# Kernel optimization log

Hardware: AMD Instinct MI355X
Metric: run time of the kernel (lower is better)

## Reference

```python
import jax, jax.numpy as jnp
import numpy as np

M, B, N, NUM_CLASSES = 3, 16, 512, 12
IOU_THR = 0.5


def setup_inputs() -> dict:
    key = jax.random.key(0)
    k1, k2, k3, k4, k5 = jax.random.split(key, 5)
    # Valid xyxy boxes in a ~1024x1024 image: x2>x1, y2>y1
    xy = jax.random.uniform(k1, (M, B, N, 2)) * 900.0
    wh = jax.random.uniform(k2, (M, B, N, 2)) * 120.0 + 4.0
    boxes = jnp.concatenate([xy, xy + wh], axis=-1)
    scores = jax.random.uniform(k3, (M, B, N))
    labels = jax.random.randint(k4, (M, B, N), 0, NUM_CLASSES)
    w = jax.random.uniform(k5, (M,)) + 0.5
    weights = w / jnp.sum(w)  # module normalizes weights to sum to 1
    return {"boxes": boxes, "scores": scores, "labels": labels, "weights": weights}


def _pairwise_iou(b):
    # b: [K,4] xyxy -> [K,K] IoU
    x1, y1, x2, y2 = b[:, 0], b[:, 1], b[:, 2], b[:, 3]
    area = (x2 - x1) * (y2 - y1)
    iw = jnp.clip(jnp.minimum(x2[:, None], x2[None, :]) - jnp.maximum(x1[:, None], x1[None, :]), 0.0)
    ih = jnp.clip(jnp.minimum(y2[:, None], y2[None, :]) - jnp.maximum(y1[:, None], y1[None, :]), 0.0)
    inter = iw * ih
    union = area[:, None] + area[None, :] - inter
    return inter / jnp.maximum(union, 1e-9)


def _nms_one_image(boxes, scores, labels):
    # boxes [K,4], scores [K], labels [K] -> [K,5] (kept boxes + kept score, suppressed rows zeroed)
    K = boxes.shape[0]
    order = jnp.argsort(-scores)  # descending score, like torchvision.ops.nms
    b = boxes[order]
    s = scores[order]
    l = labels[order]
    iou = _pairwise_iou(b)  # [K,K]
    # class-aware: only same-label boxes can suppress each other (per-label NMS loop in the original)
    suppress = (iou > IOU_THR) & (l[:, None] == l[None, :])
    idx = jnp.arange(K)
    def body(i, keep):
        # box i is suppressed iff a higher-scoring kept box of the same label overlaps > thr
        conflict = jnp.any(suppress[i] & keep & (idx < i))
        return keep.at[i].set(jnp.logical_not(conflict))
    keep = jax.lax.fori_loop(0, K, body, jnp.ones((K,), dtype=bool))
    kf = keep.astype(b.dtype)
    return jnp.concatenate([b * kf[:, None], (s * kf)[:, None]], axis=-1)


def reference(boxes, scores, labels, weights):
    # Gather all models' detections per image with score weighting, then class-aware NMS.
    K = M * N
    b = jnp.transpose(boxes, (1, 0, 2, 3)).reshape(B, K, 4)
    s = jnp.transpose(scores * weights[:, None, None], (1, 0, 2)).reshape(B, K)
    l = jnp.transpose(labels, (1, 0, 2)).reshape(B, K)
    return jax.vmap(_nms_one_image)(b, s, l)  # [B, K, 5]
```

## Files before the change

### kernel.cpp

```cpp
#include <hip/hip_runtime.h>

#define MM 3
#define BB 16
#define NN 512
#define KK 1536
#define NCLS 12
#define LMAX 256
#define LW 4
#define NTHREADS 1024
#define NWAVES 16

__global__ __launch_bounds__(NTHREADS) void nms_fused_kernel(
    const float* __restrict__ boxes, const float* __restrict__ scores,
    const int* __restrict__ labels, const float* __restrict__ weights,
    float* __restrict__ out) {
#pragma clang fp contract(off)
  int cls = blockIdx.x, b = blockIdx.y;
  int tid = threadIdx.x, lane = tid & 63, wave = tid >> 6;

  __shared__ unsigned long long kl[KK];
  __shared__ unsigned long long mkey[LMAX + 2];
  __shared__ int memb[LMAX];
  __shared__ int wcnt[NWAVES];
  __shared__ int pr[8][128];
  __shared__ float4 lb[LMAX];
  __shared__ float lsc[LMAX];
  __shared__ unsigned short listR[LMAX];
  __shared__ unsigned long long mask[LMAX][LW];
  __shared__ unsigned long long kwS[LW];

  float w0 = weights[0], w1 = weights[1], w2 = weights[2];
  bool has1 = (wave < 8);
  int t0 = wave * 64 + lane;
  int t1 = (wave + 16) * 64 + lane;
  int m0i = t0 >> 9, n0i = t0 & 511;
  float s0 = scores[(m0i * BB + b) * NN + n0i];
  int l0 = labels[(m0i * BB + b) * NN + n0i];
  float s1 = 0.0f; int l1 = -1;
  if (has1) {
    int m1i = t1 >> 9, n1i = t1 & 511;
    s1 = scores[(m1i * BB + b) * NN + n1i];
    l1 = labels[(m1i * BB + b) * NN + n1i];
  }
  unsigned long long lmask = (1ULL << lane) - 1ULL;
  float wm0 = (m0i == 0) ? w0 : ((m0i == 1) ? w1 : w2);
  unsigned long long key0 =
      ((unsigned long long)(~__float_as_uint(s0 * wm0)) << 16) | (unsigned)t0;
  kl[t0] = key0;
  bool mem0 = (l0 == cls);
  unsigned long long bk0 = __ballot(mem0);
  int off0 = __popcll(bk0 & lmask);
  int wl = __popcll(bk0);
  unsigned long long key1 = 0ULL; bool mem1 = false; int off1 = 0;
  if (has1) {
    int m1i = t1 >> 9;
    float wm1 = (m1i == 0) ? w0 : ((m1i == 1) ? w1 : w2);
    key1 = ((unsigned long long)(~__float_as_uint(s1 * wm1)) << 16) |
           (unsigned)t1;
    kl[t1] = key1;
    mem1 = (l1 == cls);
    unsigned long long bk1 = __ballot(mem1);
    off1 = wl + __popcll(bk1 & lmask);
    wl += __popcll(bk1);
  }
  if (lane == 0) wcnt[wave] = wl;
  __syncthreads();
  int wbase = 0, L = 0;
#pragma unroll
  for (int w = 0; w < NWAVES; ++w) {
    if (w < wave) wbase += wcnt[w];
    L += wcnt[w];
  }
  if (L > LMAX) L = LMAX;
  if (mem0) {
    int p = wbase + off0;
    if (p < LMAX) { memb[p] = t0; mkey[p] = key0; }
  }
  if (mem1) {
    int p = wbase + off1;
    if (p < LMAX) { memb[p] = t1; mkey[p] = key1; }
  }
  if (tid < 2) mkey[L + tid] = ~0ULL;
  __syncthreads();

  const ulonglong2* k2 = (const ulonglong2*)kl;
  const ulonglong2* m2 = (const ulonglong2*)mkey;
  int nH = (L + 1) >> 1;
  int pidx = tid & 127, s = tid >> 7;
  for (int p0 = 0; p0 < L; p0 += 128) {
    int p = p0 + pidx;
    bool own = (s == 0) && (p < L);
    unsigned long long k0 = (p < L) ? mkey[p] : ~0ULL;
    float4 box = make_float4(0.f, 0.f, 0.f, 0.f);
    if (own) {
      int e = memb[p];
      box = ((const float4*)boxes)[((e >> 9) * BB + b) * NN + (e & 511)];
    }
    int r = 0;
    const ulonglong2* ks = k2 + s * (KK / 16);
#pragma unroll 8
    for (int j = 0; j < KK / 16; ++j) {
      ulonglong2 kk = ks[j];
      r += (int)(kk.x < k0) + (int)(kk.y < k0);
    }
    pr[s][pidx] = r;
    int lp = 0;
    if (own) {
      for (int q = 0; q < nH; ++q) {
        ulonglong2 mm = m2[q];
        lp += (int)(mm.x < k0) + (int)(mm.y < k0);
      }
    }
    __syncthreads();
    if (own) {
      int grank = pr[0][pidx] + pr[1][pidx] + pr[2][pidx] + pr[3][pidx] +
                  pr[4][pidx] + pr[5][pidx] + pr[6][pidx] + pr[7][pidx];
      lb[lp] = box;
      lsc[lp] = __uint_as_float(~(unsigned)(k0 >> 16));
      listR[lp] = (unsigned short)grank;
    }
    __syncthreads();
  }

  int nWd = (L + 63) >> 6;
  for (int v = 0; v < nWd; ++v) {
    int j = v * 64 + lane;
    float4 bj = lb[min(j, L - 1)];
    float aj = (bj.z - bj.x) * (bj.w - bj.y);
    for (int i = v * 64 + wave; i < L; i += NWAVES) {
      float4 bi = lb[i];
      float ai = (bi.z - bi.x) * (bi.w - bi.y);
      float iw = fminf(bi.z, bj.z) - fmaxf(bi.x, bj.x); iw = fmaxf(iw, 0.0f);
      float ih = fminf(bi.w, bj.w) - fmaxf(bi.y, bj.y); ih = fmaxf(ih, 0.0f);
      float inter = iw * ih;
      float uni = (ai + aj) - inter;
      bool sup = (j < i) && ((double)inter > (double)uni * (0.5 + 0x1p-25));
      unsigned long long bits = __ballot(sup);
      if (lane == 0) mask[i][v] = bits;
    }
  }
  __syncthreads();

  if (wave == 0) {
    for (int w = 0; w < nWd; ++w) {
      int row = w * 64 + lane;
      unsigned long long cp = 0ULL, sup = 0ULL;
      if (row < L) {
        for (int v = 0; v < w; ++v) cp |= mask[row][v] & kwS[v];
        sup = mask[row][w];
      }
      bool conf = (cp != 0ULL);
      unsigned long long Kb = 0ULL, Sb = 0ULL;
      while (true) {
        bool kill = conf || ((sup & Kb) != 0ULL);
        bool keep = !conf && ((sup & ~Sb) == 0ULL);
        Kb = __ballot(keep);
        Sb = __ballot(kill);
        if ((Kb | Sb) == ~0ULL) break;
      }
      if (lane == 0) kwS[w] = Kb;
    }
  }
  __syncthreads();

  for (int p = tid; p < L; p += NTHREADS) {
    bool kp = (kwS[p >> 6] >> (p & 63)) & 1ULL;
    int r = listR[p];
    float* o = out + ((size_t)b * KK + r) * 5;
    if (kp) {
      float4 bx = lb[p];
      o[0] = bx.x; o[1] = bx.y; o[2] = bx.z; o[3] = bx.w; o[4] = lsc[p];
    } else {
      o[0] = 0.0f; o[1] = 0.0f; o[2] = 0.0f; o[3] = 0.0f; o[4] = 0.0f;
    }
  }
}

extern "C" void kernel_launch(void* const* d_in, const int* in_sizes, int n_in,
                              void* d_out, int out_size, void* d_ws, size_t ws_size,
                              hipStream_t stream) {
  (void)in_sizes; (void)n_in; (void)out_size; (void)d_ws; (void)ws_size;
  const float* boxes   = (const float*)d_in[0];
  const float* scores  = (const float*)d_in[1];
  const int*   labels  = (const int*)d_in[2];
  const float* weights = (const float*)d_in[3];
  float* out = (float*)d_out;

  nms_fused_kernel<<<dim3(NCLS, BB), NTHREADS, 0, stream>>>(
      boxes, scores, labels, weights, out);
}
```

Measured before the change: 75.19 us.

## Rank keys cooperatively per wave with packed shuffle reductions

Ranking is reorganised so each wave ranks 8 class members at once. Every lane compares a strided slice of the 1536 global keys, and of the padded member-key list, against all 8 keys. The per-slot counts are packed into 16-bit or 8-bit fields and summed with xor-shuffle reductions. This replaces the per-thread serial scan, the shared partial-rank array and two block barriers per pass, cutting serial loop length in the rank phase. The cost is extra shuffle and register work, and the member-key list must now be padded with sentinels all the way to its full capacity.

```diff
diff --git a/kernel.cpp b/kernel.cpp
--- a/kernel.cpp
+++ b/kernel.cpp
@@ -22,7 +22,6 @@
   __shared__ unsigned long long mkey[LMAX + 2];
   __shared__ int memb[LMAX];
   __shared__ int wcnt[NWAVES];
-  __shared__ int pr[8][128];
   __shared__ float4 lb[LMAX];
   __shared__ float lsc[LMAX];
   __shared__ unsigned short listR[LMAX];
@@ -80,47 +79,66 @@
     int p = wbase + off1;
     if (p < LMAX) { memb[p] = t1; mkey[p] = key1; }
   }
-  if (tid < 2) mkey[L + tid] = ~0ULL;
+  {
+    int x = L + tid;
+    if (x < LMAX + 2) mkey[x] = ~0ULL;
+  }
   __syncthreads();
 
   const ulonglong2* k2 = (const ulonglong2*)kl;
   const ulonglong2* m2 = (const ulonglong2*)mkey;
-  int nH = (L + 1) >> 1;
-  int pidx = tid & 127, s = tid >> 7;
-  for (int p0 = 0; p0 < L; p0 += 128) {
-    int p = p0 + pidx;
-    bool own = (s == 0) && (p < L);
-    unsigned long long k0 = (p < L) ? mkey[p] : ~0ULL;
+  int npass = (L > 128) ? 2 : 1;
+  for (int pass = 0; pass < npass; ++pass) {
+    int sbase = pass * 128 + wave * 8;
+    int slot = sbase + (lane & 7);
+    bool owner = (lane < 8) && (slot < L);
     float4 box = make_float4(0.f, 0.f, 0.f, 0.f);
-    if (own) {
-      int e = memb[p];
+    if (owner) {
+      int e = memb[slot];
       box = ((const float4*)boxes)[((e >> 9) * BB + b) * NN + (e & 511)];
     }
-    int r = 0;
-    const ulonglong2* ks = k2 + s * (KK / 16);
-#pragma unroll 8
-    for (int j = 0; j < KK / 16; ++j) {
-      ulonglong2 kk = ks[j];
-      r += (int)(kk.x < k0) + (int)(kk.y < k0);
-    }
-    pr[s][pidx] = r;
-    int lp = 0;
-    if (own) {
-      for (int q = 0; q < nH; ++q) {
-        ulonglong2 mm = m2[q];
-        lp += (int)(mm.x < k0) + (int)(mm.y < k0);
-      }
-    }
-    __syncthreads();
-    if (own) {
-      int grank = pr[0][pidx] + pr[1][pidx] + pr[2][pidx] + pr[3][pidx] +
-                  pr[4][pidx] + pr[5][pidx] + pr[6][pidx] + pr[7][pidx];
+    unsigned long long mk[8];
+#pragma unroll
+    for (int s = 0; s < 8; ++s) mk[s] = mkey[sbase + s];
+    unsigned int cnt[8] = {0, 0, 0, 0, 0, 0, 0, 0};
+#pragma unroll
+    for (int it = 0; it < 12; ++it) {
+      ulonglong2 kk = k2[it * 64 + lane];
+#pragma unroll
+      for (int s = 0; s < 8; ++s)
+        cnt[s] += (unsigned)(kk.x < mk[s]) + (unsigned)(kk.y < mk[s]);
+    }
+    ulonglong2 ma = m2[lane];
+    ulonglong2 mb = m2[64 + lane];
+    unsigned int lcn[8];
+#pragma unroll
+    for (int s = 0; s < 8; ++s)
+      lcn[s] = (unsigned)(ma.x < mk[s]) + (unsigned)(ma.y < mk[s]) +
+               (unsigned)(mb.x < mk[s]) + (unsigned)(mb.y < mk[s]);
+    unsigned int v0 = cnt[0] | (cnt[1] << 16);
+    unsigned int v1 = cnt[2] | (cnt[3] << 16);
+    unsigned int v2 = cnt[4] | (cnt[5] << 16);
+    unsigned int v3 = cnt[6] | (cnt[7] << 16);
+    unsigned int v4 = lcn[0] | (lcn[1] << 8) | (lcn[2] << 16) | (lcn[3] << 24);
+    unsigned int v5 = lcn[4] | (lcn[5] << 8) | (lcn[6] << 16) | (lcn[7] << 24);
+#pragma unroll
+    for (int d = 1; d < 64; d <<= 1) {
+      v0 += __shfl_xor((int)v0, d); v1 += __shfl_xor((int)v1, d);
+      v2 += __shfl_xor((int)v2, d); v3 += __shfl_xor((int)v3, d);
+      v4 += __shfl_xor((int)v4, d); v5 += __shfl_xor((int)v5, d);
+    }
+    if (owner) {
+      int s = lane;
+      unsigned int cw = (s < 2) ? v0 : ((s < 4) ? v1 : ((s < 6) ? v2 : v3));
+      int grank = (int)((cw >> ((s & 1) * 16)) & 0xFFFFu);
+      unsigned int lw_ = (s < 4) ? v4 : v5;
+      int lp = (int)((lw_ >> ((s & 3) * 8)) & 0xFFu);
       lb[lp] = box;
-      lsc[lp] = __uint_as_float(~(unsigned)(k0 >> 16));
+      lsc[lp] = __uint_as_float(~(unsigned)(mk[s] >> 16));
       listR[lp] = (unsigned short)grank;
     }
-    __syncthreads();
-  }
+  }
+  __syncthreads();
 
   int nWd = (L + 63) >> 6;
   for (int v = 0; v < nWd; ++v) {
```

Measured after the change: 74.32 us. About the same (-1.2%).
